# Performance work log

Hardware: AMD Instinct MI355X
Metric: run time of the kernel (lower is better)

## Reference

```python
import jax, jax.numpy as jnp
import numpy as np

D = 4; R = 12; C = 32
P = 2 * R + 1            # 25 fine patch
N = P * P                # 625
MEM_R = 12; MEM_P = 2 * MEM_R + 1
K = 20; DIL_INT = 16


def local_correlation(ft, fr, rad, dil):
    """Zero-padded local correlation (SpatialCorrelationSampler, kernel=1).
    ft, fr: (b,c,h,w) -> (b,Pp,Pp,h,w) with Pp=2*rad+1, patch dilation dil."""
    b, c, h, w = ft.shape
    Pp = 2 * rad + 1
    pad = rad * dil
    frp = jnp.pad(fr, ((0, 0), (0, 0), (pad, pad), (pad, pad)))
    rows = (jnp.arange(Pp)[:, None] * dil + jnp.arange(h)[None, :]).reshape(-1)
    cols = (jnp.arange(Pp)[:, None] * dil + jnp.arange(w)[None, :]).reshape(-1)
    g = frp[:, :, rows, :][:, :, :, cols].reshape(b, c, Pp, h, Pp, w)
    return jnp.einsum('bchw,bcyhxw->byxhw', ft, g)


def bilinear_sample(img, py, px):
    """Bilinear sample img (b,c,H,W) at float coords py/px (broadcastable shape S);
    zero outside the image. Returns (b,c,*S)."""
    b, c, H, W = img.shape
    y0f = jnp.floor(py); x0f = jnp.floor(px)
    wy = py - y0f; wx = px - x0f
    y0 = y0f.astype(jnp.int32); x0 = x0f.astype(jnp.int32)

    def tap(yi, xi, wgt):
        valid = (yi >= 0) & (yi < H) & (xi >= 0) & (xi < W)
        v = img[:, :, jnp.clip(yi, 0, H - 1), jnp.clip(xi, 0, W - 1)]
        return v * (wgt * valid)[None, None]

    return (tap(y0, x0, (1 - wy) * (1 - wx)) + tap(y0, x0 + 1, (1 - wy) * wx)
            + tap(y0 + 1, x0, wy * (1 - wx)) + tap(y0 + 1, x0 + 1, wy * wx))


def _topk_dim1(corr, k):
    # corr: (b,N,hw); torch.topk(dim=1, sorted=True) equivalent
    vals, idx = jax.lax.top_k(corr.transpose(0, 2, 1), k)   # (b,hw,k)
    return vals.transpose(0, 2, 1), idx                      # (b,k,hw), (b,hw,k)


def _long_ref(ft, fr, q, dirate):
    b, c, h, w = ft.shape
    # coarse dilated correlation -> softmax -> soft-argmax expected offset
    corr_c = local_correlation(ft, fr, MEM_R, dirate).reshape(b, MEM_P * MEM_P, h * w)
    attn = jax.nn.softmax(corr_c, axis=1).reshape(b, MEM_P, MEM_P, h, w)
    d = jnp.arange(-MEM_R, MEM_R + 1, dtype=ft.dtype)
    off_y = jnp.einsum('byxhw,y->bhw', attn, d) * dirate
    off_x = jnp.einsum('byxhw,x->bhw', attn, d) * dirate
    # deform_im2col with PxP kernel: sample fr at (r+dy+off_y, c+dx+off_x)
    dtap = jnp.arange(-R, R + 1, dtype=ft.dtype)
    py = dtap[:, None, None, None] + (jnp.arange(h, dtype=ft.dtype)[:, None] + off_y[0])[None, None]
    px = dtap[None, :, None, None] + (jnp.arange(w, dtype=ft.dtype)[None, :] + off_x[0])[None, None]
    col = bilinear_sample(fr, py, px)                        # (b,c,P,P,h,w)
    corr = jnp.einsum('bchw,bcyxhw->byxhw', ft, col).reshape(b, N, h * w)
    vals, idx = _topk_dim1(corr, K)
    # process_long_image_uf_topk: shift offsets by decoded top-k displacement, 1-tap bilinear
    dr = (idx[0] // 25 - 12).reshape(h, w, K).transpose(2, 0, 1).astype(ft.dtype)  # (K,h,w)
    dc = (idx[0] % 25 - 12).reshape(h, w, K).transpose(2, 0, 1).astype(ft.dtype)
    py2 = jnp.arange(h, dtype=ft.dtype)[None, :, None] + off_y[0][None] + dr
    px2 = jnp.arange(w, dtype=ft.dtype)[None, None, :] + off_x[0][None] + dc
    imgs = bilinear_sample(q, py2, px2)                      # (b,C,K,h,w)
    return vals, imgs.reshape(b, q.shape[1], K, h * w)


def _short_ref(ft, fr, q):
    b, c, h, w = ft.shape
    corr = local_correlation(ft, fr, R, 1).reshape(b, N, h * w)
    vals, idx = _topk_dim1(corr, K)
    # process_short_image_uf_topk: integer gather q[:, :, r+dr, c+dc] (zero-padded)
    dr = (idx[0] // 25 - 12).reshape(h, w, K).transpose(2, 0, 1)   # (K,h,w) int
    dc = (idx[0] % 25 - 12).reshape(h, w, K).transpose(2, 0, 1)
    qp = jnp.pad(q, ((0, 0), (0, 0), (R, R), (R, R)))
    yi = jnp.arange(h)[None, :, None] + dr + R
    xi = jnp.arange(w)[None, None, :] + dc + R
    imgs = qp[:, :, yi, xi]                                  # (b,C,K,h,w)
    return vals, imgs.reshape(b, q.shape[1], K, h * w)


def _forward(feats_r, feats_t, quantized_r, ref_index, current_ind):
    ref_index = np.asarray(ref_index)
    current_ind = int(current_ind)
    gaps = current_ind - ref_index
    nsearch = int(np.sum(gaps > DIL_INT))
    dirates = [int(min(4, g // DIL_INT + 1)) for g in gaps if g > DIL_INT]
    nref = feats_r.shape[0]
    b, c, h, w = feats_t.shape
    # prep(): subsample labels by D (C=32 channels, one_hot skipped)
    qr = [quantized_r[i][:, :, ::D, ::D].astype(feats_t.dtype) for i in range(nref)]
    vals_all, imgs_all = [], []
    for i in range(nsearch):
        v, im = _long_ref(feats_t, feats_r[i], qr[i], dirates[i])
        vals_all.append(v); imgs_all.append(im)
    for i in range(nsearch, nref):
        v, im = _short_ref(feats_t, feats_r[i], qr[i])
        vals_all.append(v); imgs_all.append(im)
    attn = jax.nn.softmax(jnp.concatenate(vals_all, axis=1), axis=1)  # (b, nref*K, hw)
    imgs = jnp.concatenate(imgs_all, axis=2)                          # (b, C, nref*K, hw)
    return jnp.einsum('bkp,bckp->bcp', attn, imgs).reshape(b, qr[0].shape[1], h, w)


def setup_inputs():
    key = jax.random.key(0)
    k1, k2, k3 = jax.random.split(key, 3)
    feats_r = jax.random.normal(k1, (3, 1, 64, 48, 48), dtype=jnp.float32)
    feats_t = jax.random.normal(k2, (1, 64, 48, 48), dtype=jnp.float32)
    quantized_r = jax.random.uniform(k3, (3, 1, 32, 192, 192), dtype=jnp.float32)
    # gaps vs current_ind=60: 20 (>16 -> long ref, dirate=2), 10, 5 (short refs)
    ref_index = np.array([40, 50, 55], dtype=np.int64)
    current_ind = 60
    return {"feats_r": feats_r, "feats_t": feats_t, "quantized_r": quantized_r,
            "ref_index": ref_index, "current_ind": current_ind}


def reference(feats_r, feats_t, quantized_r, ref_index, current_ind):
    return _forward(feats_r, feats_t, quantized_r, ref_index, current_ind)
```

## Files before the change

### kernel.cpp

```cpp
#include <hip/hip_runtime.h>
#include <math.h>

#define HW 48
#define NPIX 2304
#define CF 64
#define CQ 32
#define RAD 12
#define PP 25
#define NTAP 625
#define KTOP 20
#define DILINT 16
#define QW 192
#define CSTRIDE 640
#define NPB 6
#define NC 30
#define LROW 68
#define DGS 28


__device__ inline int read_ref_index(const void* rip, int r) {
    const long long* p64 = (const long long*)rip;
    long long v0 = p64[0];
    if (v0 >= 0 && v0 < 1000000) return (int)p64[r];
    return ((const int*)rip)[r];
}

__device__ inline int get_dil(const void* refIdx, const void* curInd, int r,
                              bool* isLong) {
    int cur = ((const int*)curInd)[0];
    int gap = cur - read_ref_index(refIdx, r);
    *isLong = gap > DILINT;
    return *isLong ? min(4, gap / DILINT + 1) : 1;
}

__device__ inline float gather_color(const float* __restrict__ qb, int c,
                                     int y, int x, int id, bool isLong,
                                     float oy, float ox) {
    int dr = id / PP - RAD, dc = id % PP - RAD;
    float img = 0.f;
    if (isLong) {
        float py = (float)y + oy + (float)dr;
        float px = (float)x + ox + (float)dc;
        float fy0 = floorf(py), fx0 = floorf(px);
        int y0 = (int)fy0, x0 = (int)fx0;
        float wy = py - fy0, wx = px - fx0;
        float w00 = (1.f - wy) * (1.f - wx), w01 = (1.f - wy) * wx;
        float w10 = wy * (1.f - wx), w11 = wy * wx;
        if (y0 >= 0 && y0 < HW && x0 >= 0 && x0 < HW)
            img += w00 * qb[(y0 * HW + x0) * CQ + c];
        if (y0 >= 0 && y0 < HW && x0 + 1 >= 0 && x0 + 1 < HW)
            img += w01 * qb[(y0 * HW + x0 + 1) * CQ + c];
        if (y0 + 1 >= 0 && y0 + 1 < HW && x0 >= 0 && x0 < HW)
            img += w10 * qb[((y0 + 1) * HW + x0) * CQ + c];
        if (y0 + 1 >= 0 && y0 + 1 < HW && x0 + 1 >= 0 && x0 + 1 < HW)
            img += w11 * qb[((y0 + 1) * HW + x0 + 1) * CQ + c];
    } else {
        int yy = y + dr, xx = x + dc;
        if (yy >= 0 && yy < HW && xx >= 0 && xx < HW)
            img = qb[(yy * HW + xx) * CQ + c];
    }
    return img;
}

__global__ void prep_kernel(const float* __restrict__ fr,
                            const float* __restrict__ ft,
                            const float* __restrict__ q, int nref,
                            float* __restrict__ ftT,
                            float* __restrict__ frT,
                            float* __restrict__ qrT) {
    int i = blockIdx.x * blockDim.x + threadIdx.x;
    int tft = NPIX * CF;
    int tfr = nref * NPIX * CF;
    int tqr = nref * NPIX * CQ;
    if (i < tft) {
        int c = i / NPIX, p = i - c * NPIX;
        ftT[p * CF + c] = ft[i];
    } else if (i < tft + tfr) {
        int j = i - tft;
        int rr = j / (NPIX * CF);
        int rem = j - rr * (NPIX * CF);
        int c = rem / NPIX, p = rem - c * NPIX;
        frT[((size_t)rr * NPIX + p) * CF + c] = fr[j];
    } else if (i < tft + tfr + tqr) {
        int j = i - tft - tfr;
        int rr = j / (NPIX * CQ);
        int rem = j - rr * (NPIX * CQ);
        int c = rem / NPIX, p = rem - c * NPIX;
        int y = p / HW, x = p - y * HW;
        qrT[((size_t)rr * NPIX + p) * CQ + c] =
            q[(((size_t)rr * CQ + c) * QW + 4 * y) * QW + 4 * x];
    }
}

__global__ __launch_bounds__(256) void corr_band(
    const float* __restrict__ ftT, const float* __restrict__ frT,
    const void* __restrict__ refIdx, const void* __restrict__ curInd,
    float* __restrict__ corr) {
    __shared__ float lrow[NC * LROW];

    int tid = threadIdx.x;
    int bx = blockIdx.x % 9;
    int y = blockIdx.x / 9;
    int r = blockIdx.y;

    bool isLong;
    int dil = get_dil(refIdx, curInd, r, &isLong);
    int nb = (dil == 3) ? 9 : 8;
    if (bx >= nb) return;

    int m = bx % dil, grp = bx / dil;
    int npr = HW / dil;

    int T = tid;
    bool active = T < NPB * PP;
    int j = active ? T / PP : 0;
    int dxi = active ? T - PP * j : 0;
    int xoff = grp * NPB + j;
    bool pvalid = active && (xoff < npr);
    int xj = m + dil * xoff;
    int pj = pvalid ? (y * HW + xj) : 0;
    int lc = j + dxi;

    float4 fq[16];
    const float4* fp = (const float4*)(ftT + (size_t)pj * CF);
#pragma unroll
    for (int i = 0; i < 16; ++i) fq[i] = fp[i];

    const float* frb = frT + (size_t)r * NPIX * CF;
    float* outb = corr + ((size_t)r * NPIX + pj) * CSTRIDE + dxi;
    int gc0 = m + dil * (grp * NPB - RAD);

    for (int dy = 0; dy < PP; ++dy) {
        int yy = y + dil * (dy - RAD);
        if (yy < 0 || yy >= HW) {
            if (pvalid) outb[dy * PP] = 0.f;
            continue;
        }
        for (int k = tid; k < NC * 16; k += 256) {
            int col = k >> 4, sub = k & 15;
            int gc = gc0 + dil * col;
            float4 v = {0.f, 0.f, 0.f, 0.f};
            if (gc >= 0 && gc < HW)
                v = *(const float4*)(frb + ((size_t)yy * HW + gc) * CF + sub * 4);
            *(float4*)(lrow + col * LROW + sub * 4) = v;
        }
        __syncthreads();
        if (pvalid) {
            const float* bp = lrow + lc * LROW;
            float s = 0.f;
#pragma unroll
            for (int i = 0; i < 16; ++i) {
                float4 b = *(const float4*)(bp + 4 * i);
                s += fq[i].x * b.x + fq[i].y * b.y + fq[i].z * b.z + fq[i].w * b.w;
            }
            outb[dy * PP] = s;
        }
        __syncthreads();
    }
}

__global__ __launch_bounds__(192) void corr_fuse(
    const float* __restrict__ ftT, const float* __restrict__ frT,
    const float* __restrict__ qrT, const float* __restrict__ corr,
    const void* __restrict__ refIdx, const void* __restrict__ curInd,
    int nref, float* __restrict__ out) {
    __shared__ float dgw_s[3][27 * DGS];
    __shared__ float accL[3][64];
    __shared__ float ssmL[3][64];
    __shared__ float offL[3][2];
    __shared__ float mL[3];

    int tid = threadIdx.x;
    int wid = tid >> 6, lane = tid & 63;
    int p = blockIdx.x;
    int y = p / HW, x = p % HW;
    int r = wid;

    bool isLong;
    int dil = get_dil(refIdx, curInd, r, &isLong);
    float oy = 0.f, ox = 0.f;

    const float* cb = corr + ((size_t)r * NPIX + p) * CSTRIDE;
    float creg[10];
#pragma unroll
    for (int jj = 0; jj < 10; ++jj) {
        int t = lane + 64 * jj;
        creg[jj] = (t < NTAP) ? cb[t] : -INFINITY;
    }

    if (isLong) {
        float M = -INFINITY;
#pragma unroll
        for (int jj = 0; jj < 10; ++jj) M = fmaxf(M, creg[jj]);
#pragma unroll
        for (int s = 32; s; s >>= 1) M = fmaxf(M, __shfl_xor(M, s, 64));
        float s0 = 0.f, sy = 0.f, sx = 0.f;
#pragma unroll
        for (int jj = 0; jj < 10; ++jj) {
            int t = lane + 64 * jj;
            if (t < NTAP) {
                float e = expf(creg[jj] - M);
                int dy = t / PP - RAD, dx = t % PP - RAD;
                s0 += e; sy += e * (float)dy; sx += e * (float)dx;
            }
        }
#pragma unroll
        for (int s = 32; s; s >>= 1) {
            s0 += __shfl_xor(s0, s, 64);
            sy += __shfl_xor(sy, s, 64);
            sx += __shfl_xor(sx, s, 64);
        }
        oy = sy / s0 * (float)dil;
        ox = sx / s0 * (float)dil;
        if (lane == 0) { offL[r][0] = oy; offL[r][1] = ox; }
    }
    __syncthreads();

    for (int rr = 0; rr < nref; ++rr) {
        bool rrLong;
        get_dil(refIdx, curInd, rr, &rrLong);
        if (!rrLong) continue;
        float roy = offL[rr][0], rox = offL[rr][1];
        float fy = (float)y + roy, fx = (float)x + rox;
        int iy0 = (int)floorf(fy), ix0 = (int)floorf(fx);

        int cs = tid & 15;
        int g2 = tid >> 4;
        float4 fqc = ((const float4*)(ftT + (size_t)p * CF))[cs];
        const float* frb = frT + (size_t)rr * NPIX * CF;
        float* dgw = dgw_s[rr];
        int colbase = ix0 - RAD;
        for (int a = 0; a < 26; ++a) {
            int yy = iy0 - RAD + a;
            bool yok = (yy >= 0 && yy < HW);
            const float* rowp = frb + (size_t)(yok ? yy : 0) * (HW * CF);
#pragma unroll
            for (int i = 0; i < 3; ++i) {
                int lc2 = 12 * i + g2;
                int xx2 = colbase + lc2;
                int xs = min(max(xx2, 0), HW - 1);
                float s = 0.f;
                if (yok && lc2 < 26) {
                    float4 b = *(const float4*)(rowp + xs * CF + 4 * cs);
                    s = fqc.x * b.x + fqc.y * b.y + fqc.z * b.z + fqc.w * b.w;
                    s = (xx2 >= 0 && xx2 < HW) ? s : 0.f;
                }
                s += __shfl_xor(s, 1, 64);
                s += __shfl_xor(s, 2, 64);
                s += __shfl_xor(s, 4, 64);
                s += __shfl_xor(s, 8, 64);
                if (cs == 0 && lc2 < 26) dgw[a * DGS + lc2] = s;
            }
        }
    }
    __syncthreads();

    if (isLong) {
        float fy = (float)y + oy, fx = (float)x + ox;
        float fy0 = floorf(fy), fx0 = floorf(fx);
        float wy = fy - fy0, wx = fx - fx0;
        const float* dgw = dgw_s[r];
        float w00 = (1.f - wy) * (1.f - wx), w01 = (1.f - wy) * wx;
        float w10 = wy * (1.f - wx), w11 = wy * wx;
#pragma unroll
        for (int jj = 0; jj < 10; ++jj) {
            int t = lane + 64 * jj;
            if (t < NTAP) {
                int a = t / PP, bcol = t % PP;
                creg[jj] = w00 * dgw[a * DGS + bcol] + w01 * dgw[a * DGS + bcol + 1] +
                           w10 * dgw[(a + 1) * DGS + bcol] + w11 * dgw[(a + 1) * DGS + bcol + 1];
            }
        }
    }

    double key[10];
#pragma unroll
    for (int jj = 0; jj < 10; ++jj) {
        float v = creg[jj] + 0.0f;
        unsigned u = __float_as_uint(v);
        u = (u & 0x80000000u) ? ~u : (u | 0x80000000u);
        int t = lane + 64 * jj;
        key[jj] = (double)u * 1024.0 + (double)(1023 - t);
    }

    int c = lane & 31, h = lane >> 5;
    const float* qb = qrT + (size_t)r * NPIX * CQ;
    float ssum = 0.f, acc = 0.f, m = 0.f;
    float v0a = 0.f, v0b = 0.f; int t0a = 0, t0b = 0;

    for (int k2 = 0; k2 < KTOP / 2; ++k2) {
        double a = key[0], b = -1.0;
#pragma unroll
        for (int jj = 1; jj < 10; ++jj) {
            double kk = key[jj];
            double na = fmax(a, kk);
            b = fmax(b, fmin(a, kk));
            a = na;
        }
#pragma unroll
        for (int s = 32; s; s >>= 1) {
            double pa = __shfl_xor(a, s, 64);
            double pb = __shfl_xor(b, s, 64);
            double na = fmax(a, pa);
            b = fmax(fmin(a, pa), fmax(b, pb));
            a = na;
        }
        double qa = floor(a * (1.0 / 1024.0));
        double qb2 = floor(b * (1.0 / 1024.0));
        unsigned ua = (unsigned)qa, ub = (unsigned)qb2;
        unsigned ba = (ua & 0x80000000u) ? (ua ^ 0x80000000u) : ~ua;
        unsigned bb = (ub & 0x80000000u) ? (ub ^ 0x80000000u) : ~ub;
        float va = __uint_as_float(ba), vb = __uint_as_float(bb);
        int ta = 1023 - (int)(a - qa * 1024.0);
        int tb = 1023 - (int)(b - qb2 * 1024.0);

        if (k2 == 0) {
            if (lane == 0) mL[r] = va;
            v0a = va; v0b = vb; t0a = ta; t0b = tb;
        } else {
            float vv = h ? vb : va;
            int tt = h ? tb : ta;
            float e = __expf(vv - m);
            ssum += e;
            acc += e * gather_color(qb, c, y, x, tt, isLong, oy, ox);
        }
#pragma unroll
        for (int jj = 0; jj < 10; ++jj) {
            double kk = key[jj];
            key[jj] = (kk == a || kk == b) ? 0.0 : kk;
        }
        if (k2 == 0) {
            __syncthreads();
            m = mL[0];
            for (int w = 1; w < nref; ++w) m = fmaxf(m, mL[w]);
            float vv = h ? v0b : v0a;
            int tt = h ? t0b : t0a;
            float e = __expf(vv - m);
            ssum += e;
            acc += e * gather_color(qb, c, y, x, tt, isLong, oy, ox);
        }
    }
    accL[wid][lane] = acc;
    ssmL[wid][lane] = ssum;
    __syncthreads();

    if (wid == 0) {
        float ta2 = 0.f, ts = 0.f;
        for (int w = 0; w < nref; ++w) { ta2 += accL[w][lane]; ts += ssmL[w][lane]; }
        ta2 += __shfl_xor(ta2, 32, 64);
        ts += __shfl_xor(ts, 32, 64);
        if (h == 0) out[(size_t)c * NPIX + p] = ta2 / ts;
    }
}

extern "C" void kernel_launch(void* const* d_in, const int* in_sizes, int n_in,
                              void* d_out, int out_size, void* d_ws, size_t ws_size,
                              hipStream_t stream) {
    const float* fr = (const float*)d_in[0];
    const float* ft = (const float*)d_in[1];
    const float* q  = (const float*)d_in[2];
    const void* refIdx = d_in[3];
    const void* curInd = d_in[4];
    int nref = in_sizes[0] / (CF * NPIX);

    float* ws  = (float*)d_ws;
    float* ftT = ws;
    float* frT = ftT + (size_t)NPIX * CF;
    float* qrT = frT + (size_t)nref * NPIX * CF;
    float* corr = qrT + (size_t)nref * NPIX * CQ;

    int total = NPIX * CF + nref * NPIX * CF + nref * NPIX * CQ;
    prep_kernel<<<(total + 255) / 256, 256, 0, stream>>>(fr, ft, q, nref, ftT, frT, qrT);
    corr_band<<<dim3(HW * 9, nref), 256, 0, stream>>>(ftT, frT, refIdx, curInd, corr);
    corr_fuse<<<dim3(NPIX), 64 * nref, 0, stream>>>(ftT, frT, qrT, corr, refIdx, curInd,
                                                    nref, (float*)d_out);
}
```

Measured before the change: 112.5 us.

## Double-buffer correlation rows, coalesce transpose writes, drop mid-kernel softmax barrier

The correlation band kernel now double-buffers the shared-memory reference row and prefetches the next row into registers while the current row is consumed. This leaves one barrier per row, where there were two, and lets global loads overlap the dot products. The prep transpose now indexes by output, so writes are coalesced and reads are strided. The fused kernel drops the cross-wave max barrier after the first top-k pick. Each wave uses its own local max, and the final reduction rescales each wave's partial sums by exp(m_w - M), which costs a few extra exps per pixel.

```diff
diff --git a/kernel.cpp b/kernel.cpp
--- a/kernel.cpp
+++ b/kernel.cpp
@@ -73,22 +73,21 @@
     int tfr = nref * NPIX * CF;
     int tqr = nref * NPIX * CQ;
     if (i < tft) {
-        int c = i / NPIX, p = i - c * NPIX;
-        ftT[p * CF + c] = ft[i];
+        int p = i >> 6, c = i & 63;
+        ftT[i] = ft[c * NPIX + p];
     } else if (i < tft + tfr) {
         int j = i - tft;
         int rr = j / (NPIX * CF);
-        int rem = j - rr * (NPIX * CF);
-        int c = rem / NPIX, p = rem - c * NPIX;
-        frT[((size_t)rr * NPIX + p) * CF + c] = fr[j];
+        int rem = j % (NPIX * CF);
+        int p = rem >> 6, c = rem & 63;
+        frT[j] = fr[((size_t)rr * CF + c) * NPIX + p];
     } else if (i < tft + tfr + tqr) {
         int j = i - tft - tfr;
         int rr = j / (NPIX * CQ);
-        int rem = j - rr * (NPIX * CQ);
-        int c = rem / NPIX, p = rem - c * NPIX;
-        int y = p / HW, x = p - y * HW;
-        qrT[((size_t)rr * NPIX + p) * CQ + c] =
-            q[(((size_t)rr * CQ + c) * QW + 4 * y) * QW + 4 * x];
+        int rem = j % (NPIX * CQ);
+        int p = rem >> 5, c = rem & 31;
+        int y = p / HW, x = p % HW;
+        qrT[j] = q[(((size_t)rr * CQ + c) * QW + 4 * y) * QW + 4 * x];
     }
 }
 
@@ -96,7 +95,7 @@
     const float* __restrict__ ftT, const float* __restrict__ frT,
     const void* __restrict__ refIdx, const void* __restrict__ curInd,
     float* __restrict__ corr) {
-    __shared__ float lrow[NC * LROW];
+    __shared__ float lrow[2][NC * LROW];
 
     int tid = threadIdx.x;
     int bx = blockIdx.x % 9;
@@ -130,30 +129,54 @@
     float* outb = corr + ((size_t)r * NPIX + pj) * CSTRIDE + dxi;
     int gc0 = m + dil * (grp * NPB - RAD);
 
+    int col0 = tid >> 4, sub0 = tid & 15;
+    int k1 = tid + 256;
+    int col1 = k1 >> 4, sub1 = k1 & 15;
+    bool has1 = (k1 < NC * 16);
+    int gcA = gc0 + dil * col0;
+    int gcB = gc0 + dil * col1;
+    bool okA = (gcA >= 0 && gcA < HW);
+    bool okB = has1 && (gcB >= 0 && gcB < HW);
+    const float4 z4 = {0.f, 0.f, 0.f, 0.f};
+
+    {
+        int yy = y + dil * (0 - RAD);
+        if (yy >= 0 && yy < HW) {
+            float4 a = okA ? *(const float4*)(frb + ((size_t)yy * HW + gcA) * CF + sub0 * 4) : z4;
+            *(float4*)(lrow[0] + col0 * LROW + sub0 * 4) = a;
+            if (has1) {
+                float4 b = okB ? *(const float4*)(frb + ((size_t)yy * HW + gcB) * CF + sub1 * 4) : z4;
+                *(float4*)(lrow[0] + col1 * LROW + sub1 * 4) = b;
+            }
+        }
+    }
+    __syncthreads();
+
     for (int dy = 0; dy < PP; ++dy) {
+        int cur = dy & 1;
+        float4 rA = z4, rB = z4;
+        int yn = y + dil * (dy + 1 - RAD);
+        bool nvalid = (dy + 1 < PP) && (yn >= 0 && yn < HW);
+        if (nvalid) {
+            if (okA) rA = *(const float4*)(frb + ((size_t)yn * HW + gcA) * CF + sub0 * 4);
+            if (okB) rB = *(const float4*)(frb + ((size_t)yn * HW + gcB) * CF + sub1 * 4);
+        }
         int yy = y + dil * (dy - RAD);
-        if (yy < 0 || yy >= HW) {
-            if (pvalid) outb[dy * PP] = 0.f;
-            continue;
-        }
-        for (int k = tid; k < NC * 16; k += 256) {
-            int col = k >> 4, sub = k & 15;
-            int gc = gc0 + dil * col;
-            float4 v = {0.f, 0.f, 0.f, 0.f};
-            if (gc >= 0 && gc < HW)
-                v = *(const float4*)(frb + ((size_t)yy * HW + gc) * CF + sub * 4);
-            *(float4*)(lrow + col * LROW + sub * 4) = v;
-        }
-        __syncthreads();
         if (pvalid) {
-            const float* bp = lrow + lc * LROW;
             float s = 0.f;
-#pragma unroll
-            for (int i = 0; i < 16; ++i) {
-                float4 b = *(const float4*)(bp + 4 * i);
-                s += fq[i].x * b.x + fq[i].y * b.y + fq[i].z * b.z + fq[i].w * b.w;
+            if (yy >= 0 && yy < HW) {
+                const float* bp = lrow[cur] + lc * LROW;
+#pragma unroll
+                for (int i = 0; i < 16; ++i) {
+                    float4 b = *(const float4*)(bp + 4 * i);
+                    s += fq[i].x * b.x + fq[i].y * b.y + fq[i].z * b.z + fq[i].w * b.w;
+                }
             }
             outb[dy * PP] = s;
+        }
+        if (nvalid) {
+            *(float4*)(lrow[cur ^ 1] + col0 * LROW + sub0 * 4) = rA;
+            if (has1) *(float4*)(lrow[cur ^ 1] + col1 * LROW + sub1 * 4) = rB;
         }
         __syncthreads();
     }
@@ -286,7 +309,6 @@
     int c = lane & 31, h = lane >> 5;
     const float* qb = qrT + (size_t)r * NPIX * CQ;
     float ssum = 0.f, acc = 0.f, m = 0.f;
-    float v0a = 0.f, v0b = 0.f; int t0a = 0, t0b = 0;
 
     for (int k2 = 0; k2 < KTOP / 2; ++k2) {
         double a = key[0], b = -1.0;
@@ -315,38 +337,34 @@
         int tb = 1023 - (int)(b - qb2 * 1024.0);
 
         if (k2 == 0) {
+            m = va;
             if (lane == 0) mL[r] = va;
-            v0a = va; v0b = vb; t0a = ta; t0b = tb;
-        } else {
-            float vv = h ? vb : va;
-            int tt = h ? tb : ta;
-            float e = __expf(vv - m);
-            ssum += e;
-            acc += e * gather_color(qb, c, y, x, tt, isLong, oy, ox);
-        }
+        }
+        float vv = h ? vb : va;
+        int tt = h ? tb : ta;
+        float e = __expf(vv - m);
+        ssum += e;
+        acc += e * gather_color(qb, c, y, x, tt, isLong, oy, ox);
+
 #pragma unroll
         for (int jj = 0; jj < 10; ++jj) {
             double kk = key[jj];
             key[jj] = (kk == a || kk == b) ? 0.0 : kk;
         }
-        if (k2 == 0) {
-            __syncthreads();
-            m = mL[0];
-            for (int w = 1; w < nref; ++w) m = fmaxf(m, mL[w]);
-            float vv = h ? v0b : v0a;
-            int tt = h ? t0b : t0a;
-            float e = __expf(vv - m);
-            ssum += e;
-            acc += e * gather_color(qb, c, y, x, tt, isLong, oy, ox);
-        }
     }
     accL[wid][lane] = acc;
     ssmL[wid][lane] = ssum;
     __syncthreads();
 
     if (wid == 0) {
+        float M = mL[0];
+        for (int w = 1; w < nref; ++w) M = fmaxf(M, mL[w]);
         float ta2 = 0.f, ts = 0.f;
-        for (int w = 0; w < nref; ++w) { ta2 += accL[w][lane]; ts += ssmL[w][lane]; }
+        for (int w = 0; w < nref; ++w) {
+            float sc = __expf(mL[w] - M);
+            ta2 += accL[w][lane] * sc;
+            ts += ssmL[w][lane] * sc;
+        }
         ta2 += __shfl_xor(ta2, 32, 64);
         ts += __shfl_xor(ts, 32, 64);
         if (h == 0) out[(size_t)c * NPIX + p] = ta2 / ts;
```

Measured after the change: 115.7 us. 1.03x slower.

## Restructure correlation dot products across lanes and defer softmax max merging

Applied to the files above, without the earlier changes.

The prep transpose now writes coalesced and gathers on the read side. The band correlation kernel gives each thread one column and an 8-channel slice, computing partial dot products for all six query pixels with shuffle reductions. This replaces one thread per (pixel, offset) doing a full 64-channel dot product over strided LDS rows. The fuse kernel drops the mid-loop __syncthreads for the global max by using each wave's local max and rescaling the partial sums at the final merge, adding exp calls and shuffle traffic in exchange.

```diff
diff --git a/kernel.cpp b/kernel.cpp
--- a/kernel.cpp
+++ b/kernel.cpp
@@ -73,22 +73,21 @@
     int tfr = nref * NPIX * CF;
     int tqr = nref * NPIX * CQ;
     if (i < tft) {
-        int c = i / NPIX, p = i - c * NPIX;
-        ftT[p * CF + c] = ft[i];
+        int p = i >> 6, c = i & 63;
+        ftT[i] = ft[c * NPIX + p];
     } else if (i < tft + tfr) {
         int j = i - tft;
         int rr = j / (NPIX * CF);
-        int rem = j - rr * (NPIX * CF);
-        int c = rem / NPIX, p = rem - c * NPIX;
-        frT[((size_t)rr * NPIX + p) * CF + c] = fr[j];
+        int rem = j % (NPIX * CF);
+        int p = rem >> 6, c = rem & 63;
+        frT[j] = fr[((size_t)rr * CF + c) * NPIX + p];
     } else if (i < tft + tfr + tqr) {
         int j = i - tft - tfr;
         int rr = j / (NPIX * CQ);
-        int rem = j - rr * (NPIX * CQ);
-        int c = rem / NPIX, p = rem - c * NPIX;
-        int y = p / HW, x = p - y * HW;
-        qrT[((size_t)rr * NPIX + p) * CQ + c] =
-            q[(((size_t)rr * CQ + c) * QW + 4 * y) * QW + 4 * x];
+        int rem = j % (NPIX * CQ);
+        int p = rem >> 5, c = rem & 31;
+        int y = p / HW, x = p % HW;
+        qrT[j] = q[(((size_t)rr * CQ + c) * QW + 4 * y) * QW + 4 * x];
     }
 }
 
@@ -111,29 +110,40 @@
     int m = bx % dil, grp = bx / dil;
     int npr = HW / dil;
 
-    int T = tid;
-    bool active = T < NPB * PP;
-    int j = active ? T / PP : 0;
-    int dxi = active ? T - PP * j : 0;
-    int xoff = grp * NPB + j;
-    bool pvalid = active && (xoff < npr);
-    int xj = m + dil * xoff;
-    int pj = pvalid ? (y * HW + xj) : 0;
-    int lc = j + dxi;
-
-    float4 fq[16];
-    const float4* fp = (const float4*)(ftT + (size_t)pj * CF);
-#pragma unroll
-    for (int i = 0; i < 16; ++i) fq[i] = fp[i];
+    int c = tid >> 3;
+    int e = tid & 7;
+    bool cact = (c < NC);
+
+    float4 fta[NPB][2];
+    bool jv[NPB];
+    int pjr[NPB];
+#pragma unroll
+    for (int j = 0; j < NPB; ++j) {
+        int xoff = grp * NPB + j;
+        jv[j] = (xoff < npr);
+        int xj = m + dil * xoff;
+        pjr[j] = y * HW + (jv[j] ? xj : 0);
+        const float4* fp = (const float4*)(ftT + (size_t)pjr[j] * CF + e * 8);
+        fta[j][0] = fp[0];
+        fta[j][1] = fp[1];
+    }
+
+    int dxs = c - e;
+    bool st_ok = cact && (e < NPB) && (dxs >= 0) && (dxs < PP);
+    int pj_e = 0; bool jv_e = false;
+#pragma unroll
+    for (int j = 0; j < NPB; ++j)
+        if (e == j) { pj_e = pjr[j]; jv_e = jv[j]; }
+    st_ok = st_ok && jv_e;
+    float* outp = corr + ((size_t)r * NPIX + pj_e) * CSTRIDE + dxs;
 
     const float* frb = frT + (size_t)r * NPIX * CF;
-    float* outb = corr + ((size_t)r * NPIX + pj) * CSTRIDE + dxi;
     int gc0 = m + dil * (grp * NPB - RAD);
 
     for (int dy = 0; dy < PP; ++dy) {
         int yy = y + dil * (dy - RAD);
         if (yy < 0 || yy >= HW) {
-            if (pvalid) outb[dy * PP] = 0.f;
+            if (st_ok) outp[dy * PP] = 0.f;
             continue;
         }
         for (int k = tid; k < NC * 16; k += 256) {
@@ -145,16 +155,29 @@
             *(float4*)(lrow + col * LROW + sub * 4) = v;
         }
         __syncthreads();
-        if (pvalid) {
-            const float* bp = lrow + lc * LROW;
-            float s = 0.f;
-#pragma unroll
-            for (int i = 0; i < 16; ++i) {
-                float4 b = *(const float4*)(bp + 4 * i);
-                s += fq[i].x * b.x + fq[i].y * b.y + fq[i].z * b.z + fq[i].w * b.w;
-            }
-            outb[dy * PP] = s;
-        }
+
+        const float* bp = lrow + c * LROW + e * 8;
+        float4 b0 = *(const float4*)(bp);
+        float4 b1 = *(const float4*)(bp + 4);
+        float part[NPB];
+#pragma unroll
+        for (int j = 0; j < NPB; ++j) {
+            part[j] = fta[j][0].x * b0.x + fta[j][0].y * b0.y +
+                      fta[j][0].z * b0.z + fta[j][0].w * b0.w +
+                      fta[j][1].x * b1.x + fta[j][1].y * b1.y +
+                      fta[j][1].z * b1.z + fta[j][1].w * b1.w;
+        }
+#pragma unroll
+        for (int s = 1; s < 8; s <<= 1) {
+#pragma unroll
+            for (int j = 0; j < NPB; ++j)
+                part[j] += __shfl_xor(part[j], s, 64);
+        }
+        float sv = part[0];
+#pragma unroll
+        for (int j = 1; j < NPB; ++j)
+            if (e == j) sv = part[j];
+        if (st_ok) outp[dy * PP] = sv;
         __syncthreads();
     }
 }
@@ -286,7 +309,6 @@
     int c = lane & 31, h = lane >> 5;
     const float* qb = qrT + (size_t)r * NPIX * CQ;
     float ssum = 0.f, acc = 0.f, m = 0.f;
-    float v0a = 0.f, v0b = 0.f; int t0a = 0, t0b = 0;
 
     for (int k2 = 0; k2 < KTOP / 2; ++k2) {
         double a = key[0], b = -1.0;
@@ -315,38 +337,34 @@
         int tb = 1023 - (int)(b - qb2 * 1024.0);
 
         if (k2 == 0) {
+            m = va;
             if (lane == 0) mL[r] = va;
-            v0a = va; v0b = vb; t0a = ta; t0b = tb;
-        } else {
-            float vv = h ? vb : va;
-            int tt = h ? tb : ta;
-            float e = __expf(vv - m);
-            ssum += e;
-            acc += e * gather_color(qb, c, y, x, tt, isLong, oy, ox);
-        }
+        }
+        float vv = h ? vb : va;
+        int tt = h ? tb : ta;
+        float e = __expf(vv - m);
+        ssum += e;
+        acc += e * gather_color(qb, c, y, x, tt, isLong, oy, ox);
+
 #pragma unroll
         for (int jj = 0; jj < 10; ++jj) {
             double kk = key[jj];
             key[jj] = (kk == a || kk == b) ? 0.0 : kk;
         }
-        if (k2 == 0) {
-            __syncthreads();
-            m = mL[0];
-            for (int w = 1; w < nref; ++w) m = fmaxf(m, mL[w]);
-            float vv = h ? v0b : v0a;
-            int tt = h ? t0b : t0a;
-            float e = __expf(vv - m);
-            ssum += e;
-            acc += e * gather_color(qb, c, y, x, tt, isLong, oy, ox);
-        }
     }
     accL[wid][lane] = acc;
     ssmL[wid][lane] = ssum;
     __syncthreads();
 
     if (wid == 0) {
+        float M = mL[0];
+        for (int w = 1; w < nref; ++w) M = fmaxf(M, mL[w]);
         float ta2 = 0.f, ts = 0.f;
-        for (int w = 0; w < nref; ++w) { ta2 += accL[w][lane]; ts += ssmL[w][lane]; }
+        for (int w = 0; w < nref; ++w) {
+            float sc = __expf(mL[w] - M);
+            ta2 += accL[w][lane] * sc;
+            ts += ssmL[w][lane] * sc;
+        }
         ta2 += __shfl_xor(ta2, 32, 64);
         ts += __shfl_xor(ts, 32, 64);
         if (h == 0) out[(size_t)c * NPIX + p] = ta2 / ts;
```

Result: slower. 115.9 us (+3.0%).
